# Kernel tuning notes

Hardware: AMD Instinct MI355X
Metric: run time of the kernel (lower is better)

## Reference

```python
import jax, jax.numpy as jnp
import numpy as np

EPS = 1e-12  # F.normalize clamp eps
LOGIT_SCALE = float(np.exp(np.log(100.0)))  # coattn_logit_scale.exp() == 100.0


def _l2norm(x):
    n = jnp.linalg.norm(x, axis=-1, keepdims=True)
    return x / jnp.maximum(n, EPS)


def setup_inputs() -> dict:
    key = jax.random.key(0)
    k1, k2, k3, k4 = jax.random.split(key, 4)
    B, N, C = 1, 100000, 1024
    NUM_QUERY = 10  # +1 gated query
    X = jax.random.normal(k1, (B, N, C), dtype=jnp.float32)
    Q = jax.random.normal(k2, (NUM_QUERY + 1, C), dtype=jnp.float32)
    W = jax.random.normal(k3, (C, C), dtype=jnp.float32) * (1.0 / np.sqrt(C))
    b = jax.random.normal(k4, (C,), dtype=jnp.float32) * 0.01
    return {"X": X, "Q": Q, "W": W, "b": b}


def reference(X, Q, W, b):
    # X: [1, N, C] bag features; Q: [num_query+1, C]; W,b: visual_adapter Linear
    Qn = _l2norm(Q)[None]            # [1, q+1, C]
    Xn = _l2norm(X)                  # [1, N, C]
    A_ = jnp.einsum('bqc,bnc->bqn', Qn, Xn)   # cosine similarities [1, q+1, N]
    # gated-query subtraction: last query's scores subtracted from the rest
    A_ = A_[:, :-1, :] - A_[:, -1:, :]        # [1, q, N]
    A = jax.nn.softmax(LOGIT_SCALE * A_, axis=-1)
    out = jnp.einsum('bqn,bnc->bqc', A, X)    # [1, q, C]
    pooled = jnp.mean(out, axis=1)            # 'mean' query pooling -> [1, C]
    return pooled @ W.T + b                   # visual_adapter (nn.Linear)
```

## Files before the change

kernel.cpp:

```cpp
#include <hip/hip_runtime.h>
#include <float.h>
#include <math.h>

#define C     1024
#define NQ    10
#define G4    512
#define NPAIR (G4 * 2)

template <int CTRL, int ROWM>
__device__ __forceinline__ float dpp_add(float x) {
  int mv = __builtin_amdgcn_update_dpp(0, __float_as_int(x), CTRL, ROWM, 0xf, true);
  return x + __int_as_float(mv);
}
__device__ __forceinline__ float wave_sum64(float x) {
  x = dpp_add<0xB1,  0xf>(x);
  x = dpp_add<0x4E,  0xf>(x);
  x = dpp_add<0x141, 0xf>(x);
  x = dpp_add<0x140, 0xf>(x);
  x = dpp_add<0x142, 0xa>(x);
  x = dpp_add<0x143, 0xc>(x);
  return __int_as_float(__builtin_amdgcn_readlane(__float_as_int(x), 63));
}

__device__ __forceinline__ void scale4(float4& v, float s) {
  v.x *= s; v.y *= s; v.z *= s; v.w *= s;
}
__device__ __forceinline__ void fma4(float4& acc, float w, const float4& x) {
  acc.x = fmaf(w, x.x, acc.x); acc.y = fmaf(w, x.y, acc.y);
  acc.z = fmaf(w, x.z, acc.z); acc.w = fmaf(w, x.w, acc.w);
}

__global__ __launch_bounds__(256) void k0_qdiff(const float* __restrict__ Q,
                                                float* __restrict__ qd) {
  __shared__ float red[256];
  __shared__ float inorm[NQ + 1];
  int t = threadIdx.x;
  for (int k = 0; k <= NQ; ++k) {
    float s = 0.f;
    for (int c = t; c < C; c += 256) { float v = Q[k * C + c]; s = fmaf(v, v, s); }
    red[t] = s; __syncthreads();
    for (int st = 128; st > 0; st >>= 1) {
      if (t < st) red[t] += red[t + st];
      __syncthreads();
    }
    if (t == 0) inorm[k] = 1.0f / fmaxf(sqrtf(red[0]), 1e-12f);
    __syncthreads();
  }
  for (int k = 0; k < NQ; ++k)
    for (int c = t; c < C; c += 256)
      qd[k * C + c] = Q[k * C + c] * inorm[k] - Q[NQ * C + c] * inorm[NQ];
}

__global__ __launch_bounds__(256, 2) void kf_fused(const float* __restrict__ X,
                                                   const float* __restrict__ qd,
                                                   float* __restrict__ partial,
                                                   float* __restrict__ dsum,
                                                   float* __restrict__ mblk,
                                                   int N) {
  const int t = threadIdx.x;
  const int l = t & 63, wv = t >> 6;
  const int pr = wv >> 1;
  const int qbase = (wv & 1) * 5;
  const int co = l << 2;
  const int pid = blockIdx.x * 2 + pr;

  float4 q4[5][4];
#pragma unroll
  for (int k = 0; k < 5; ++k)
#pragma unroll
    for (int j = 0; j < 4; ++j)
      q4[k][j] = *(const float4*)(qd + (qbase + k) * C + j * 256 + co);

  float4 a[5][4];
  float ds[5], mo[5];
#pragma unroll
  for (int k = 0; k < 5; ++k) {
    a[k][0] = a[k][1] = a[k][2] = a[k][3] = make_float4(0.f, 0.f, 0.f, 0.f);
    ds[k] = 0.f; mo[k] = -FLT_MAX;
  }

#pragma unroll 1
  for (int r = pid; r < N; r += NPAIR) {
    const float* xp = X + (size_t)r * C + co;
    float4 xv[4];
#pragma unroll
    for (int j = 0; j < 4; ++j) xv[j] = *(const float4*)(xp + j * 256);

    float ss = 0.f;
    float dt[5];
#pragma unroll
    for (int k = 0; k < 5; ++k) dt[k] = 0.f;
#pragma unroll
    for (int j = 0; j < 4; ++j) {
      float4 v = xv[j];
      ss = fmaf(v.x, v.x, fmaf(v.y, v.y, fmaf(v.z, v.z, fmaf(v.w, v.w, ss))));
#pragma unroll
      for (int k = 0; k < 5; ++k) {
        float4 q = q4[k][j];
        dt[k] = fmaf(v.x, q.x, fmaf(v.y, q.y, fmaf(v.z, q.z, fmaf(v.w, q.w, dt[k]))));
      }
    }
    float rn = 100.0f / fmaxf(sqrtf(wave_sum64(ss)), 1e-12f);
#pragma unroll
    for (int k = 0; k < 5; ++k) {
      float lg = wave_sum64(dt[k]) * rn;
      float mn = fmaxf(mo[k], lg);
      if (mn > mo[k]) {
        float sc = __expf(mo[k] - mn);
        ds[k] *= sc;
        scale4(a[k][0], sc); scale4(a[k][1], sc);
        scale4(a[k][2], sc); scale4(a[k][3], sc);
        mo[k] = mn;
      }
      float w = __expf(lg - mo[k]);
      ds[k] += w;
      fma4(a[k][0], w, xv[0]); fma4(a[k][1], w, xv[1]);
      fma4(a[k][2], w, xv[2]); fma4(a[k][3], w, xv[3]);
    }
  }

  __shared__ float wm[4][8];
  __shared__ float wd[4][8];
  __shared__ float part[NQ][C];
  if (l == 0) {
#pragma unroll
    for (int k = 0; k < 5; ++k) { wm[wv][k] = mo[k]; wd[wv][k] = ds[k]; }
  }
  __syncthreads();
  float sc[5];
#pragma unroll
  for (int k = 0; k < 5; ++k) {
    float M = fmaxf(wm[wv][k], wm[wv ^ 2][k]);
    sc[k] = __expf(mo[k] - M);
  }
  if (wv < 2) {
#pragma unroll
    for (int k = 0; k < 5; ++k)
#pragma unroll
      for (int j = 0; j < 4; ++j) {
        float4 o = a[k][j]; scale4(o, sc[k]);
        *(float4*)&part[qbase + k][j * 256 + co] = o;
      }
  }
  __syncthreads();
  if (wv >= 2) {
#pragma unroll
    for (int k = 0; k < 5; ++k)
#pragma unroll
      for (int j = 0; j < 4; ++j) {
        float4 p = *(const float4*)&part[qbase + k][j * 256 + co];
        float4 o = a[k][j];
        p.x = fmaf(o.x, sc[k], p.x); p.y = fmaf(o.y, sc[k], p.y);
        p.z = fmaf(o.z, sc[k], p.z); p.w = fmaf(o.w, sc[k], p.w);
        *(float4*)&part[qbase + k][j * 256 + co] = p;
      }
  }
  __syncthreads();

  {
    const float4* src = (const float4*)&part[0][0];
    float4* dst = (float4*)&partial[(size_t)blockIdx.x * NQ * C];
    for (int idx = t; idx < NQ * (C / 4); idx += 256) dst[idx] = src[idx];
  }
  if (t < NQ) {
    int w0 = (t < 5) ? 0 : 1, k5 = (t < 5) ? t : t - 5;
    float m0 = wm[w0][k5], m1 = wm[w0 + 2][k5];
    float M = fmaxf(m0, m1);
    dsum[blockIdx.x * NQ + t] =
        wd[w0][k5] * __expf(m0 - M) + wd[w0 + 2][k5] * __expf(m1 - M);
    mblk[blockIdx.x * 16 + t] = M;
  }
}

__global__ __launch_bounds__(256) void k5a_pooled(const float* __restrict__ partial,
                                                  const float* __restrict__ dsum,
                                                  const float* __restrict__ mblk,
                                                  float* __restrict__ pooled) {
  __shared__ float sM[16], sF[16];
  __shared__ float red[256];
  __shared__ float r4[256][4];
  int t = threadIdx.x;
  int k = t & 15, grp = t >> 4;

  float mm = -FLT_MAX;
  if (k < NQ)
    for (int g = grp; g < G4; g += 16) mm = fmaxf(mm, mblk[g * 16 + k]);
  red[t] = mm; __syncthreads();
  if (t < 16) {
    float m2 = red[t];
    for (int j = 1; j < 16; ++j) m2 = fmaxf(m2, red[t + 16 * j]);
    sM[t] = m2;
  }
  __syncthreads();

  float dd = 0.f;
  if (k < NQ) {
    float Mk = sM[k];
    for (int g = grp; g < G4; g += 16)
      dd += dsum[g * NQ + k] * __expf(mblk[g * 16 + k] - Mk);
  }
  red[t] = dd; __syncthreads();
  if (t < 16) {
    float d2 = 0.f;
    for (int j = 0; j < 16; ++j) d2 += red[t + 16 * j];
    sF[t] = 1.0f / ((float)NQ * d2);
  }
  __syncthreads();

  int c0 = blockIdx.x * 4;
  float a0 = 0.f, a1 = 0.f, a2 = 0.f, a3 = 0.f;
  for (int idx = t; idx < G4 * NQ; idx += 256) {
    int g = idx / NQ, kq = idx - g * NQ;
    float f = __expf(mblk[g * 16 + kq] - sM[kq]) * sF[kq];
    const float4 p = *(const float4*)&partial[(((size_t)idx) << 10) + c0];
    a0 = fmaf(p.x, f, a0); a1 = fmaf(p.y, f, a1);
    a2 = fmaf(p.z, f, a2); a3 = fmaf(p.w, f, a3);
  }
  r4[t][0] = a0; r4[t][1] = a1; r4[t][2] = a2; r4[t][3] = a3;
  __syncthreads();
  for (int st = 128; st > 0; st >>= 1) {
    if (t < st) {
      r4[t][0] += r4[t + st][0]; r4[t][1] += r4[t + st][1];
      r4[t][2] += r4[t + st][2]; r4[t][3] += r4[t + st][3];
    }
    __syncthreads();
  }
  if (t < 4) pooled[c0 + t] = r4[0][t];
}

__global__ __launch_bounds__(256) void k5b_out(const float* __restrict__ W,
                                               const float* __restrict__ bias,
                                               const float* __restrict__ pooled,
                                               float* __restrict__ out) {
  __shared__ float sp[C];
  int t = threadIdx.x;
  for (int i = t; i < C; i += 256) sp[i] = pooled[i];
  __syncthreads();
  int wv = t >> 6, lane = t & 63;
#pragma unroll
  for (int jj = 0; jj < 8; ++jj) {
    int j = blockIdx.x * 32 + wv * 8 + jj;
    float s = 0.f;
#pragma unroll
    for (int seg = 0; seg < 4; ++seg) {
      int cbase = seg * 256 + lane * 4;
      float4 w4 = *(const float4*)&W[(size_t)j * C + cbase];
      float4 p4 = *(const float4*)&sp[cbase];
      s += w4.x * p4.x + w4.y * p4.y + w4.z * p4.z + w4.w * p4.w;
    }
#pragma unroll
    for (int off = 32; off > 0; off >>= 1) s += __shfl_down(s, off);
    if (lane == 0) out[j] = s + bias[j];
  }
}

extern "C" void kernel_launch(void* const* d_in, const int* in_sizes, int n_in,
                              void* d_out, int out_size, void* d_ws, size_t ws_size,
                              hipStream_t stream) {
  const float* X = (const float*)d_in[0];
  const float* Q = (const float*)d_in[1];
  const float* W = (const float*)d_in[2];
  const float* b = (const float*)d_in[3];
  float* out = (float*)d_out;

  int N = in_sizes[0] / C;

  float* ws      = (float*)d_ws;
  float* qd      = ws;
  float* mblk    = qd + NQ * C;
  float* dsum    = mblk + G4 * 16;
  float* pooled  = dsum + G4 * NQ;
  float* partial = pooled + C;

  hipLaunchKernelGGL(k0_qdiff,  dim3(1),      dim3(256), 0, stream, Q, qd);
  hipLaunchKernelGGL(kf_fused,  dim3(G4),     dim3(256), 0, stream,
                     X, qd, partial, dsum, mblk, N);
  hipLaunchKernelGGL(k5a_pooled,dim3(C / 4),  dim3(256), 0, stream,
                     partial, dsum, mblk, pooled);
  hipLaunchKernelGGL(k5b_out,   dim3(C / 32), dim3(256), 0, stream, W, b, pooled, out);
}
```

Measured before the change: 650.9 us.

## Fuse query normalization into main kernel and double-row load in stream loop

```diff
diff --git a/kernel.cpp b/kernel.cpp
--- a/kernel.cpp
+++ b/kernel.cpp
@@ -30,29 +30,8 @@
   acc.z = fmaf(w, x.z, acc.z); acc.w = fmaf(w, x.w, acc.w);
 }
 
-__global__ __launch_bounds__(256) void k0_qdiff(const float* __restrict__ Q,
-                                                float* __restrict__ qd) {
-  __shared__ float red[256];
-  __shared__ float inorm[NQ + 1];
-  int t = threadIdx.x;
-  for (int k = 0; k <= NQ; ++k) {
-    float s = 0.f;
-    for (int c = t; c < C; c += 256) { float v = Q[k * C + c]; s = fmaf(v, v, s); }
-    red[t] = s; __syncthreads();
-    for (int st = 128; st > 0; st >>= 1) {
-      if (t < st) red[t] += red[t + st];
-      __syncthreads();
-    }
-    if (t == 0) inorm[k] = 1.0f / fmaxf(sqrtf(red[0]), 1e-12f);
-    __syncthreads();
-  }
-  for (int k = 0; k < NQ; ++k)
-    for (int c = t; c < C; c += 256)
-      qd[k * C + c] = Q[k * C + c] * inorm[k] - Q[NQ * C + c] * inorm[NQ];
-}
-
 __global__ __launch_bounds__(256, 2) void kf_fused(const float* __restrict__ X,
-                                                   const float* __restrict__ qd,
+                                                   const float* __restrict__ Q,
                                                    float* __restrict__ partial,
                                                    float* __restrict__ dsum,
                                                    float* __restrict__ mblk,
@@ -65,11 +44,36 @@
   const int pid = blockIdx.x * 2 + pr;
 
   float4 q4[5][4];
-#pragma unroll
-  for (int k = 0; k < 5; ++k)
-#pragma unroll
-    for (int j = 0; j < 4; ++j)
-      q4[k][j] = *(const float4*)(qd + (qbase + k) * C + j * 256 + co);
+  {
+    float4 qn[4];
+    float ssn = 0.f;
+#pragma unroll
+    for (int j = 0; j < 4; ++j) {
+      qn[j] = *(const float4*)(Q + NQ * C + j * 256 + co);
+      ssn = fmaf(qn[j].x, qn[j].x, fmaf(qn[j].y, qn[j].y,
+            fmaf(qn[j].z, qn[j].z, fmaf(qn[j].w, qn[j].w, ssn))));
+    }
+    const float inN = 1.0f / fmaxf(sqrtf(wave_sum64(ssn)), 1e-12f);
+#pragma unroll
+    for (int k = 0; k < 5; ++k) {
+      float4 qf[4];
+      float ssq = 0.f;
+#pragma unroll
+      for (int j = 0; j < 4; ++j) {
+        qf[j] = *(const float4*)(Q + (qbase + k) * C + j * 256 + co);
+        ssq = fmaf(qf[j].x, qf[j].x, fmaf(qf[j].y, qf[j].y,
+              fmaf(qf[j].z, qf[j].z, fmaf(qf[j].w, qf[j].w, ssq))));
+      }
+      const float ink = 1.0f / fmaxf(sqrtf(wave_sum64(ssq)), 1e-12f);
+#pragma unroll
+      for (int j = 0; j < 4; ++j) {
+        q4[k][j].x = qf[j].x * ink - qn[j].x * inN;
+        q4[k][j].y = qf[j].y * ink - qn[j].y * inN;
+        q4[k][j].z = qf[j].z * ink - qn[j].z * inN;
+        q4[k][j].w = qf[j].w * ink - qn[j].w * inN;
+      }
+    }
+  }
 
   float4 a[5][4];
   float ds[5], mo[5];
@@ -79,13 +83,7 @@
     ds[k] = 0.f; mo[k] = -FLT_MAX;
   }
 
-#pragma unroll 1
-  for (int r = pid; r < N; r += NPAIR) {
-    const float* xp = X + (size_t)r * C + co;
-    float4 xv[4];
-#pragma unroll
-    for (int j = 0; j < 4; ++j) xv[j] = *(const float4*)(xp + j * 256);
-
+  auto proc = [&](const float4 (&xv)[4]) {
     float ss = 0.f;
     float dt[5];
 #pragma unroll
@@ -117,6 +115,25 @@
       fma4(a[k][0], w, xv[0]); fma4(a[k][1], w, xv[1]);
       fma4(a[k][2], w, xv[2]); fma4(a[k][3], w, xv[3]);
     }
+  };
+
+#pragma unroll 1
+  for (int r = pid; r < N; r += 2 * NPAIR) {
+    const int r2 = r + NPAIR;
+    const bool two = (r2 < N);
+    float4 x0[4], x1[4];
+    {
+      const float* xp = X + (size_t)r * C + co;
+#pragma unroll
+      for (int j = 0; j < 4; ++j) x0[j] = *(const float4*)(xp + j * 256);
+    }
+    if (two) {
+      const float* xp = X + (size_t)r2 * C + co;
+#pragma unroll
+      for (int j = 0; j < 4; ++j) x1[j] = *(const float4*)(xp + j * 256);
+    }
+    proc(x0);
+    if (two) proc(x1);
   }
 
   __shared__ float wm[4][8];
@@ -266,15 +283,13 @@
   int N = in_sizes[0] / C;
 
   float* ws      = (float*)d_ws;
-  float* qd      = ws;
-  float* mblk    = qd + NQ * C;
+  float* mblk    = ws;
   float* dsum    = mblk + G4 * 16;
   float* pooled  = dsum + G4 * NQ;
   float* partial = pooled + C;
 
-  hipLaunchKernelGGL(k0_qdiff,  dim3(1),      dim3(256), 0, stream, Q, qd);
   hipLaunchKernelGGL(kf_fused,  dim3(G4),     dim3(256), 0, stream,
-                     X, qd, partial, dsum, mblk, N);
+                     X, Q, partial, dsum, mblk, N);
   hipLaunchKernelGGL(k5a_pooled,dim3(C / 4),  dim3(256), 0, stream,
                      partial, dsum, mblk, pooled);
   hipLaunchKernelGGL(k5b_out,   dim3(C / 32), dim3(256), 0, stream, W, b, pooled, out);
```

After: 603.4 us. 1.08x faster.
